# Kernel tuning notes

Hardware: AMD Instinct MI355X
Metric: run time of the kernel (lower is better)

The kernel has to match this reference:

```python
import jax, jax.numpy as jnp
import numpy as np

B, S, D, H, L = 4, 4096, 64, 8, 4
VOCAB, NCLS = 256, 10
MLP = D * H          # mlp_dim = dim * heads = 512
BS = 256             # block size for banded attention
R = 256              # one-sided radius (sliding_window_size = 512)


def sinusoid_pos_emb(s, d):
    pos = np.arange(s)[:, None].astype(np.float32)
    i = np.arange(d // 2)[None, :].astype(np.float32)
    ang = pos / np.power(10000.0, 2.0 * i / d)
    pe = np.zeros((s, d), np.float32)
    pe[:, 0::2] = np.sin(ang)
    pe[:, 1::2] = np.cos(ang)
    return jnp.asarray(pe)


def layernorm(x, s, b):
    m = x.mean(-1, keepdims=True)
    v = ((x - m) ** 2).mean(-1, keepdims=True)
    return (x - m) * jax.lax.rsqrt(v + 1e-6) * s + b


def sliding_window_attn(x, wq, bq, wk, bk, wv, bv, wo, bo):
    Bx, Sx, Dx = x.shape
    Dh = Dx // H
    nb = Sx // BS

    def proj(w, b2):
        return (x @ w + b2).reshape(Bx, Sx, H, Dh).transpose(0, 2, 1, 3)

    q = proj(wq, bq) / jnp.sqrt(jnp.float32(Dh))
    k = proj(wk, bk)
    v = proj(wv, bv)

    def windows(t):  # [B,H,S,Dh] -> [B,H,nb,3*BS,Dh] (prev | self | next blocks)
        tp = jnp.pad(t, ((0, 0), (0, 0), (BS, BS), (0, 0))).reshape(Bx, H, nb + 2, BS, Dh)
        return jnp.concatenate([tp[:, :, :-2], tp[:, :, 1:-1], tp[:, :, 2:]], axis=3)

    kw, vw = windows(k), windows(v)
    qb = q.reshape(Bx, H, nb, BS, Dh)
    scores = jnp.einsum('bhnqd,bhnkd->bhnqk', qb, kw)      # [B,H,nb,BS,3*BS]

    qpos = jnp.arange(BS)[:, None]
    kpos = jnp.arange(3 * BS)[None, :] - BS
    band = jnp.abs(kpos - qpos) <= R                        # [BS,3*BS]
    kglob = jnp.arange(nb)[:, None, None] * BS + kpos[None]  # [nb,1,3*BS]
    valid = (kglob >= 0) & (kglob < Sx)
    mask = band[None] & valid                                # [nb,BS,3*BS]

    scores = jnp.where(mask[None, None], scores, jnp.float32(-1e30))
    probs = jax.nn.softmax(scores, axis=-1)
    out = jnp.einsum('bhnqk,bhnkd->bhnqd', probs, vw)
    out = out.reshape(Bx, H, Sx, Dh).transpose(0, 2, 1, 3).reshape(Bx, Sx, Dx)
    return out @ wo + bo


def setup_inputs() -> dict:
    key = jax.random.key(0)
    ks = jax.random.split(key, 12)
    g = lambda k, shp: jax.random.normal(k, shp, dtype=jnp.float32) * 0.02
    emb = g(ks[0], (VOCAB, D)).at[0].set(0.0)  # padding_idx=0 row is zeros
    return dict(
        x=jax.random.randint(ks[1], (B, S), 0, VOCAB).astype(jnp.int32),
        emb=emb,
        wq=g(ks[2], (L, D, D)), bq=jnp.zeros((L, D)),
        wk=g(ks[3], (L, D, D)), bk=jnp.zeros((L, D)),
        wv=g(ks[4], (L, D, D)), bv=jnp.zeros((L, D)),
        wo=g(ks[5], (L, D, D)), bo=jnp.zeros((L, D)),
        ln1_s=jnp.ones((L, D)), ln1_b=jnp.zeros((L, D)),
        ln2_s=jnp.ones((L, D)), ln2_b=jnp.zeros((L, D)),
        w1=g(ks[6], (L, D, MLP)), b1=jnp.zeros((L, MLP)),
        w2=g(ks[7], (L, MLP, D)), b2=jnp.zeros((L, D)),
        lnf_s=jnp.ones((D,)), lnf_b=jnp.zeros((D,)),
        wcls=g(ks[8], (D, NCLS)), bcls=jnp.zeros((NCLS,)),
    )


def reference(x, emb, wq, bq, wk, bk, wv, bv, wo, bo, ln1_s, ln1_b, ln2_s, ln2_b, w1, b1, w2, b2, lnf_s, lnf_b, wcls, bcls):
    h = emb[x] + sinusoid_pos_emb(S, D)[None]                 # embedding + fixed pos emb
    for l in range(L):
        a = sliding_window_attn(layernorm(h, ln1_s[l], ln1_b[l]),
                                wq[l], bq[l], wk[l], bk[l], wv[l], bv[l], wo[l], bo[l])
        h = h + a
        y = layernorm(h, ln2_s[l], ln2_b[l])
        y = jax.nn.gelu(y @ w1[l] + b1[l]) @ w2[l] + b2[l]
        h = h + y
    h = layernorm(h, lnf_s, lnf_b)
    pooled = h.mean(axis=1)                                   # classifier_pool='MEAN'
    return pooled @ wcls + bcls
```

## Files before the change

### kernel.cpp

```cpp
#include <hip/hip_runtime.h>
#include <hip/hip_bf16.h>

#define DEV __device__ __forceinline__

typedef __attribute__((ext_vector_type(8))) short bf16x8;
typedef __attribute__((ext_vector_type(4))) float f32x4;
typedef __attribute__((ext_vector_type(16))) float f32x16;

DEV short f2bf(float x){ __hip_bfloat16 h = __float2bfloat16(x); return *(short*)&h; }
DEV unsigned pack2bf(float a, float b){
  return (unsigned)(unsigned short)f2bf(a) | ((unsigned)(unsigned short)f2bf(b) << 16);
}
DEV float gelu_fast(float x){
  float z = 0.7978845608028654f*(x + 0.044715f*x*x*x);
  float e = __expf(-2.f*z);
  return x / (1.f + e);
}

#define SB 4096
#define DM 64
#define VSTR 664

__global__ __launch_bounds__(256) void wconv(
    const float* __restrict__ wq, const float* __restrict__ wk,
    const float* __restrict__ wv, const float* __restrict__ wo,
    const float* __restrict__ w1, const float* __restrict__ w2,
    short* __restrict__ wqT, short* __restrict__ wkT,
    short* __restrict__ wvT, short* __restrict__ woT,
    short* __restrict__ w1T, short* __restrict__ w2T)
{
  int t = blockIdx.x, l = blockIdx.y;
  const float* src; short* dst; int K, N, kt, nt;
  if (t < 16) {
    int m = t >> 2, sub = t & 3; kt = sub >> 1; nt = sub & 1; K = 64; N = 64;
    const float* s4[4] = {wq, wk, wv, wo};
    short*       d4[4] = {wqT, wkT, wvT, woT};
    src = s4[m] + l*4096; dst = d4[m] + l*4096;
  } else if (t < 48) {
    kt = (t-16) >> 4; nt = (t-16) & 15; K = 64; N = 512;
    src = w1 + l*32768; dst = w1T + l*32768;
  } else {
    kt = (t-48) >> 1; nt = (t-48) & 1; K = 512; N = 64;
    src = w2 + l*32768; dst = w2T + l*32768;
  }
  __shared__ float lds[32][33];
  int tx = threadIdx.x & 31, ty = threadIdx.x >> 5;
  int k0 = kt*32, n0 = nt*32;
  #pragma unroll
  for (int j=0;j<4;++j) lds[ty+8*j][tx] = src[(size_t)(k0+ty+8*j)*N + n0 + tx];
  __syncthreads();
  #pragma unroll
  for (int j=0;j<4;++j) {
    int nn = ty+8*j;
    dst[(size_t)(n0+nn)*K + k0 + tx] = f2bf(lds[tx][nn]);
  }
}

DEV void make_frags_ln(const float* rowp, float mean, float inv,
    const float* __restrict__ s, const float* __restrict__ b, int kq,
    bf16x8& a0, bf16x8& a1){
  #pragma unroll
  for (int i=0;i<8;++i) a0[i] = f2bf((rowp[kq*8+i]-mean)*inv*s[kq*8+i]+b[kq*8+i]);
  #pragma unroll
  for (int i=0;i<8;++i) a1[i] = f2bf((rowp[32+kq*8+i]-mean)*inv*s[32+kq*8+i]+b[32+kq*8+i]);
}

template<bool EMBED, bool LAST>
__global__ __launch_bounds__(512,2) void fused_kernel(
    const int* __restrict__ x, const float* __restrict__ emb,
    const unsigned short* __restrict__ ab,
    const short* __restrict__ woT, const float* __restrict__ bo,
    const float* __restrict__ ln2s, const float* __restrict__ ln2b,
    const short* __restrict__ w1T, const float* __restrict__ b1,
    const short* __restrict__ w2T, const float* __restrict__ b2,
    const float* __restrict__ lns, const float* __restrict__ lnb,
    const short* __restrict__ wqT, const short* __restrict__ wkT, const short* __restrict__ wvT,
    const float* __restrict__ bq, const float* __restrict__ bk, const float* __restrict__ bv,
    unsigned short* __restrict__ qo, unsigned short* __restrict__ ko, unsigned short* __restrict__ vo,
    float* __restrict__ h, float* __restrict__ part)
{
  __shared__ float hN[64][68];
  __shared__ short mid[64][520];
  __shared__ float facc[64][68];
  __shared__ float mu[64], iv[64];

  const int bid = blockIdx.x;
  const int row_g0 = bid * 64;
  const int tid = threadIdx.x;
  const int w = tid >> 6, lane = tid & 63;
  const int r = lane & 15, kq = lane >> 4;
  const int srow = tid >> 3, sd8 = tid & 7;

  if constexpr (EMBED) {
    int tg = row_g0 + srow;
    int s = tg & (SB-1);
    int tok = x[tg];
    #pragma unroll
    for (int i=0;i<8;++i) {
      int d = sd8*8 + i;
      float fe = (float)(d & ~1) * (1.0f/64.0f);
      float invk = __expf(-9.210340371976184f * fe);
      float ang = (float)s * invk;
      float pe = (d & 1) ? __cosf(ang) : __sinf(ang);
      float val = emb[tok*DM + d] + pe;
      hN[srow][d] = val;
      h[(size_t)tg*DM + d] = val;
    }
  } else {
    const int rh = w >> 2, ct = w & 3;
    const int col = ct*16 + r;
    const short* wp = woT + (size_t)col*64 + kq*8;
    bf16x8 wb0 = *(const bf16x8*)(wp);
    bf16x8 wb1 = *(const bf16x8*)(wp + 32);
    #pragma unroll
    for (int rf=0; rf<2; ++rf) {
      const short* abp = (const short*)(ab + (size_t)(row_g0 + rh*32 + rf*16 + r)*DM + kq*8);
      bf16x8 a0 = *(const bf16x8*)abp;
      bf16x8 a1 = *(const bf16x8*)(abp + 32);
      f32x4 acc = (f32x4){0.f,0.f,0.f,0.f};
      acc = __builtin_amdgcn_mfma_f32_16x16x32_bf16(a0, wb0, acc, 0, 0, 0);
      acc = __builtin_amdgcn_mfma_f32_16x16x32_bf16(a1, wb1, acc, 0, 0, 0);
      #pragma unroll
      for (int j=0;j<4;++j) {
        int rl = rh*32 + rf*16 + kq*4 + j;
        hN[rl][col] = acc[j] + bo[col] + h[(size_t)(row_g0+rl)*DM + col];
      }
    }
  }
  __syncthreads();

  {
    const float* p = &hN[srow][sd8*8];
    float v[8];
    float sum = 0.f;
    #pragma unroll
    for (int i=0;i<8;++i){ v[i] = p[i]; sum += v[i]; }
    sum += __shfl_xor(sum, 1, 64); sum += __shfl_xor(sum, 2, 64); sum += __shfl_xor(sum, 4, 64);
    float mean = sum * (1.f/64.f);
    float sq = 0.f;
    #pragma unroll
    for (int i=0;i<8;++i){ float d = v[i]-mean; sq += d*d; }
    sq += __shfl_xor(sq, 1, 64); sq += __shfl_xor(sq, 2, 64); sq += __shfl_xor(sq, 4, 64);
    if (sd8 == 0) { mu[srow] = mean; iv[srow] = rsqrtf(sq*(1.f/64.f) + 1e-6f); }
  }
  __syncthreads();

  if constexpr (!EMBED) {
    {
      bf16x8 a[4][2];
      #pragma unroll
      for (int rf=0; rf<4; ++rf)
        make_frags_ln(&hN[rf*16 + r][0], mu[rf*16 + r], iv[rf*16 + r], ln2s, ln2b, kq, a[rf][0], a[rf][1]);
      const int gc0 = w*64;
      bf16x8 wb[4][2];
      #pragma unroll
      for (int ct=0; ct<4; ++ct) {
        const short* wp = w1T + (size_t)(gc0 + ct*16 + r)*64 + kq*8;
        wb[ct][0] = *(const bf16x8*)(wp);
        wb[ct][1] = *(const bf16x8*)(wp + 32);
      }
      f32x4 acc1[4][4];
      #pragma unroll
      for (int ct=0;ct<4;++ct)
        #pragma unroll
        for (int rf=0;rf<4;++rf) acc1[ct][rf] = (f32x4){0.f,0.f,0.f,0.f};
      #pragma unroll
      for (int ct=0; ct<4; ++ct)
        #pragma unroll
        for (int rf=0; rf<4; ++rf) {
          acc1[ct][rf] = __builtin_amdgcn_mfma_f32_16x16x32_bf16(a[rf][0], wb[ct][0], acc1[ct][rf], 0, 0, 0);
          acc1[ct][rf] = __builtin_amdgcn_mfma_f32_16x16x32_bf16(a[rf][1], wb[ct][1], acc1[ct][rf], 0, 0, 0);
        }
      #pragma unroll
      for (int ct=0; ct<4; ++ct) {
        int gcol = gc0 + ct*16 + r;
        float bb = b1[gcol];
        #pragma unroll
        for (int rf=0; rf<4; ++rf)
          #pragma unroll
          for (int j=0; j<4; ++j)
            mid[rf*16 + kq*4 + j][gcol] = f2bf(gelu_fast(acc1[ct][rf][j] + bb));
      }
    }
    __syncthreads();

    {
      const int kh = w >> 2, ct2 = w & 3;
      const int col2 = ct2*16 + r;
      bf16x8 wf[8];
      #pragma unroll
      for (int ks=0; ks<8; ++ks)
        wf[ks] = *(const bf16x8*)(w2T + (size_t)col2*512 + kh*256 + ks*32 + kq*8);
      f32x4 acc2[4];
      #pragma unroll
      for (int rf=0;rf<4;++rf) acc2[rf] = (f32x4){0.f,0.f,0.f,0.f};
      #pragma unroll
      for (int ks=0; ks<8; ++ks)
        #pragma unroll
        for (int rf=0; rf<4; ++rf) {
          bf16x8 af = *(const bf16x8*)(&mid[rf*16 + r][kh*256 + ks*32 + kq*8]);
          acc2[rf] = __builtin_amdgcn_mfma_f32_16x16x32_bf16(af, wf[ks], acc2[rf], 0, 0, 0);
        }
      if (kh == 0) {
        #pragma unroll
        for (int rf=0; rf<4; ++rf)
          #pragma unroll
          for (int j=0;j<4;++j)
            facc[rf*16 + kq*4 + j][col2] = acc2[rf][j];
      }
      __syncthreads();
      if (kh == 1) {
        float bb = b2[col2];
        #pragma unroll
        for (int rf=0; rf<4; ++rf)
          #pragma unroll
          for (int j=0;j<4;++j) {
            int rl = rf*16 + kq*4 + j;
            float val = acc2[rf][j] + facc[rl][col2] + bb + hN[rl][col2];
            hN[rl][col2] = val;
            h[(size_t)(row_g0+rl)*DM + col2] = val;
          }
      }
    }
    __syncthreads();

    {
      const float* p = &hN[srow][sd8*8];
      float v[8];
      float sum = 0.f;
      #pragma unroll
      for (int i=0;i<8;++i){ v[i] = p[i]; sum += v[i]; }
      sum += __shfl_xor(sum, 1, 64); sum += __shfl_xor(sum, 2, 64); sum += __shfl_xor(sum, 4, 64);
      float mean = sum * (1.f/64.f);
      float sq = 0.f;
      #pragma unroll
      for (int i=0;i<8;++i){ float d = v[i]-mean; sq += d*d; }
      sq += __shfl_xor(sq, 1, 64); sq += __shfl_xor(sq, 2, 64); sq += __shfl_xor(sq, 4, 64);
      if (sd8 == 0) { mu[srow] = mean; iv[srow] = rsqrtf(sq*(1.f/64.f) + 1e-6f); }
    }
    __syncthreads();
  }

  if constexpr (!LAST) {
    const float qscale = 0.35355339059327373f;
    bf16x8 a[4][2];
    #pragma unroll
    for (int rf=0; rf<4; ++rf)
      make_frags_ln(&hN[rf*16 + r][0], mu[rf*16 + r], iv[rf*16 + r], lns, lnb, kq, a[rf][0], a[rf][1]);
    #pragma unroll
    for (int rep=0; rep<2; ++rep) {
      int jj = w + rep*8;
      if (jj < 12) {
        int m = jj >> 2, ct = jj & 3;
        const short* WT = m==0 ? wqT : (m==1 ? wkT : wvT);
        int col = ct*16 + r;
        const short* wp = WT + (size_t)col*64 + kq*8;
        bf16x8 wb0 = *(const bf16x8*)(wp);
        bf16x8 wb1 = *(const bf16x8*)(wp + 32);
        float bias = (m==0 ? bq : (m==1 ? bk : bv))[col];
        float scale = (m==0) ? qscale : 1.f;
        unsigned short* OPT = m==0 ? qo : (m==1 ? ko : vo);
        #pragma unroll
        for (int rf=0; rf<4; ++rf) {
          f32x4 acc = (f32x4){0.f,0.f,0.f,0.f};
          acc = __builtin_amdgcn_mfma_f32_16x16x32_bf16(a[rf][0], wb0, acc, 0, 0, 0);
          acc = __builtin_amdgcn_mfma_f32_16x16x32_bf16(a[rf][1], wb1, acc, 0, 0, 0);
          #pragma unroll
          for (int j=0;j<4;++j) {
            size_t oi = (size_t)(row_g0 + rf*16 + kq*4 + j)*DM + col;
            OPT[oi] = (unsigned short)f2bf((acc[j] + bias)*scale);
          }
        }
      }
    }
  } else {
    float mean = mu[srow], inv = iv[srow];
    #pragma unroll
    for (int i=0;i<8;++i) {
      int d = sd8*8 + i;
      hN[srow][d] = (hN[srow][d]-mean)*inv*lns[d] + lnb[d];
    }
    __syncthreads();
    if (tid < 64) {
      float s = 0.f;
      #pragma unroll 4
      for (int rr=0; rr<64; ++rr) s += hN[rr][tid];
      part[bid*64 + tid] = s;
    }
  }
}

__global__ __launch_bounds__(256) void attn_kernel(
    const unsigned short* __restrict__ qg_,
    const unsigned short* __restrict__ kg_,
    const unsigned short* __restrict__ vg_,
    __hip_bfloat16* __restrict__ out)
{
  const int qblk = blockIdx.x, bh = blockIdx.y;
  const int b = bh >> 3, hh = bh & 7;
  const int tid = threadIdx.x;
  const int q0b = qblk << 7;
  const int kbase = q0b - 256;

  __shared__ unsigned short Ks[640*8];
  __shared__ unsigned short Vs[8*VSTR];

  const unsigned short* kgp = kg_ + ((size_t)b*SB)*DM + hh*8;
  const unsigned short* vgp = vg_ + ((size_t)b*SB)*DM + hh*8;

  for (int e = tid; e < 640; e += 256) {
    int g = kbase + e;
    uint4 kv = make_uint4(0,0,0,0), vv = make_uint4(0,0,0,0);
    if ((unsigned)g < (unsigned)SB) {
      kv = *(const uint4*)(kgp + (size_t)g*DM);
      vv = *(const uint4*)(vgp + (size_t)g*DM);
    }
    *(uint4*)(Ks + e*8) = kv;
    const unsigned short* pv = (const unsigned short*)&vv;
    #pragma unroll
    for (int d = 0; d < 8; ++d) Vs[d*VSTR + e] = pv[d];
  }
  __syncthreads();

  const int w = tid >> 6;
  const int lane = tid & 63;
  const int qc = lane & 31;
  const int hf = lane >> 5;
  const int qglob = q0b + 32*w + qc;

  bf16x8 qfrag = {};
  if (hf == 0) qfrag = *(const bf16x8*)(qg_ + ((size_t)b*SB + qglob)*DM + hh*8);

  f32x16 oacc = {};
  float lacc = 0.f;

  for (int t = 0; t <= 16; ++t) {
    const int k0l = 32*w + 32*t;
    const int k0g = kbase + k0l;
    if (k0g > SB-1 || k0g + 31 < 0) continue;

    bf16x8 kfrag = {};
    if (hf == 0) kfrag = *(const bf16x8*)(Ks + (k0l + qc)*8);

    f32x16 s = __builtin_amdgcn_mfma_f32_32x32x16_bf16(kfrag, qfrag, (f32x16){}, 0, 0, 0);

    float pp[16];
    bool needmask = (t == 0) | (t == 16) | (k0g < 0) | (k0g + 31 > SB-1);
    if (needmask) {
      #pragma unroll
      for (int rr = 0; rr < 16; ++rr) {
        int klg = k0g + (rr&3) + 8*(rr>>2) + 4*hf;
        bool ok = ((unsigned)(klg - qglob + 256) <= 512u) && ((unsigned)klg < (unsigned)SB);
        pp[rr] = ok ? __expf(s[rr]) : 0.f;
      }
    } else {
      #pragma unroll
      for (int rr = 0; rr < 16; ++rr) pp[rr] = __expf(s[rr]);
    }
    #pragma unroll
    for (int rr = 0; rr < 16; ++rr) lacc += pp[rr];

    unsigned pk[8];
    #pragma unroll
    for (int j = 0; j < 8; ++j) pk[j] = pack2bf(pp[2*j], pp[2*j+1]);
    unsigned sw[8];
    #pragma unroll
    for (int j = 0; j < 8; ++j) sw[j] = __shfl_xor(pk[j], 32, 64);

    union { unsigned u[4]; bf16x8 v; } pb1;
    pb1.u[0] = hf ? sw[2] : pk[0];
    pb1.u[1] = hf ? sw[3] : pk[1];
    pb1.u[2] = hf ? pk[2] : sw[0];
    pb1.u[3] = hf ? pk[3] : sw[1];
    bf16x8 va1 = {};
    if (qc < 8) va1 = *(const bf16x8*)(Vs + qc*VSTR + k0l + 8*hf);
    oacc = __builtin_amdgcn_mfma_f32_32x32x16_bf16(va1, pb1.v, oacc, 0, 0, 0);

    union { unsigned u[4]; bf16x8 v; } pb2;
    pb2.u[0] = hf ? sw[6] : pk[4];
    pb2.u[1] = hf ? sw[7] : pk[5];
    pb2.u[2] = hf ? pk[6] : sw[4];
    pb2.u[3] = hf ? pk[7] : sw[5];
    bf16x8 va2 = {};
    if (qc < 8) va2 = *(const bf16x8*)(Vs + qc*VSTR + k0l + 16 + 8*hf);
    oacc = __builtin_amdgcn_mfma_f32_32x32x16_bf16(va2, pb2.v, oacc, 0, 0, 0);
  }

  float lsum = lacc + __shfl_xor(lacc, 32, 64);
  float rcp = 1.f / lsum;
  unsigned short ov[4];
  #pragma unroll
  for (int j = 0; j < 4; ++j) ov[j] = (unsigned short)f2bf(oacc[j] * rcp);
  *(uint2*)(out + ((size_t)b*SB + qglob)*DM + hh*8 + 4*hf) = *(uint2*)ov;
}

__global__ __launch_bounds__(256) void pool_finalize(const float* __restrict__ part,
    const float* __restrict__ wcls, const float* __restrict__ bcls, float* __restrict__ out)
{
  int tid = threadIdx.x;
  int b = tid >> 6, d = tid & 63;
  float sum = 0.f;
  #pragma unroll 8
  for (int i = 0; i < 64; ++i) sum += part[(b*64 + i)*64 + d];
  __shared__ float pooled[4][64];
  pooled[b][d] = sum * (1.f/4096.f);
  __syncthreads();
  if (tid < 40) {
    int bb = tid / 10, c = tid % 10;
    float acc = bcls[c];
    #pragma unroll
    for (int dd = 0; dd < 64; ++dd) acc = fmaf(pooled[bb][dd], wcls[dd*10 + c], acc);
    out[tid] = acc;
  }
}

extern "C" void kernel_launch(void* const* d_in, const int* in_sizes, int n_in,
                              void* d_out, int out_size, void* d_ws, size_t ws_size,
                              hipStream_t stream)
{
  const int*   x    = (const int*)d_in[0];
  const float* emb  = (const float*)d_in[1];
  const float* wq   = (const float*)d_in[2];
  const float* bq   = (const float*)d_in[3];
  const float* wk   = (const float*)d_in[4];
  const float* bk   = (const float*)d_in[5];
  const float* wv   = (const float*)d_in[6];
  const float* bv   = (const float*)d_in[7];
  const float* wo   = (const float*)d_in[8];
  const float* bo   = (const float*)d_in[9];
  const float* ln1s = (const float*)d_in[10];
  const float* ln1b = (const float*)d_in[11];
  const float* ln2s = (const float*)d_in[12];
  const float* ln2b = (const float*)d_in[13];
  const float* w1   = (const float*)d_in[14];
  const float* b1   = (const float*)d_in[15];
  const float* w2   = (const float*)d_in[16];
  const float* b2   = (const float*)d_in[17];
  const float* lnfs = (const float*)d_in[18];
  const float* lnfb = (const float*)d_in[19];
  const float* wcls = (const float*)d_in[20];
  const float* bcls = (const float*)d_in[21];
  float* out = (float*)d_out;

  char* wsb = (char*)d_ws;
  const size_t MB = 1u << 20;
  float* h  = (float*)(wsb);
  unsigned short* qb2 = (unsigned short*)(wsb + 4*MB);
  unsigned short* kb2 = (unsigned short*)(wsb + 6*MB);
  unsigned short* vb2 = (unsigned short*)(wsb + 8*MB);
  unsigned short* ab  = (unsigned short*)(wsb + 10*MB);
  short* wqT = (short*)(wsb + 12*MB);
  short* wkT = (short*)(wsb + 12*MB + 32*1024);
  short* wvT = (short*)(wsb + 12*MB + 64*1024);
  short* woT = (short*)(wsb + 12*MB + 96*1024);
  short* w1T = (short*)(wsb + 12*MB + 128*1024);
  short* w2T = (short*)(wsb + 12*MB + 384*1024);
  float* part = (float*)(wsb + 13*MB);

  wconv<<<dim3(80,4),256,0,stream>>>(wq,wk,wv,wo,w1,w2, wqT,wkT,wvT,woT,w1T,w2T);

  fused_kernel<true,false><<<256,512,0,stream>>>(
      x, emb, nullptr,
      nullptr, nullptr, nullptr, nullptr,
      nullptr, nullptr, nullptr, nullptr,
      ln1s, ln1b,
      wqT, wkT, wvT, bq, bk, bv,
      qb2, kb2, vb2, h, nullptr);

  for (int l = 0; l < 4; ++l) {
    attn_kernel<<<dim3(32,32),256,0,stream>>>(qb2, kb2, vb2, (__hip_bfloat16*)ab);
    if (l < 3) {
      fused_kernel<false,false><<<256,512,0,stream>>>(
          nullptr, nullptr, ab,
          woT+4096*l, bo+64*l, ln2s+64*l, ln2b+64*l,
          w1T+32768*l, b1+512*l, w2T+32768*l, b2+64*l,
          ln1s+64*(l+1), ln1b+64*(l+1),
          wqT+4096*(l+1), wkT+4096*(l+1), wvT+4096*(l+1),
          bq+64*(l+1), bk+64*(l+1), bv+64*(l+1),
          qb2, kb2, vb2, h, nullptr);
    } else {
      fused_kernel<false,true><<<256,512,0,stream>>>(
          nullptr, nullptr, ab,
          woT+4096*l, bo+64*l, ln2s+64*l, ln2b+64*l,
          w1T+32768*l, b1+512*l, w2T+32768*l, b2+64*l,
          lnfs, lnfb,
          nullptr, nullptr, nullptr, nullptr, nullptr, nullptr,
          nullptr, nullptr, nullptr, h, part);
    }
  }
  pool_finalize<<<1,256,0,stream>>>(part, wcls, bcls, out);
}
```

Baseline: 204.3 us.

## Fuse sliding-window attention into the per-layer fused kernel with ping-pong QKV buffers

Removes the separate attention kernel and computes banded attention for each 64-row tile inside the layer kernel. Each block loads a 576-row K/V window for all 8 heads into shared memory, and each wave handles one head. The attention output stays in LDS and feeds the output projection directly, so the global round-trip through the attention buffer and one launch per layer are gone. Q/K/V are double-buffered across layers to avoid read/write hazards. The cost is reused LDS regions, an extra barrier, and only 256 blocks of work that each recompute a wide K/V window, which lowers parallelism for the attention part.

```diff
diff --git a/kernel.cpp b/kernel.cpp
--- a/kernel.cpp
+++ b/kernel.cpp
@@ -18,8 +18,8 @@
 }
 
 #define SB 4096
+#define NT 16384
 #define DM 64
-#define VSTR 664
 
 __global__ __launch_bounds__(256) void wconv(
     const float* __restrict__ wq, const float* __restrict__ wk,
@@ -66,9 +66,10 @@
 }
 
 template<bool EMBED, bool LAST>
-__global__ __launch_bounds__(512,2) void fused_kernel(
+__global__ __launch_bounds__(512,2) void layer_kernel(
     const int* __restrict__ x, const float* __restrict__ emb,
-    const unsigned short* __restrict__ ab,
+    const unsigned short* __restrict__ qin, const unsigned short* __restrict__ kin,
+    const unsigned short* __restrict__ vin,
     const short* __restrict__ woT, const float* __restrict__ bo,
     const float* __restrict__ ln2s, const float* __restrict__ ln2b,
     const short* __restrict__ w1T, const float* __restrict__ b1,
@@ -79,10 +80,16 @@
     unsigned short* __restrict__ qo, unsigned short* __restrict__ ko, unsigned short* __restrict__ vo,
     float* __restrict__ h, float* __restrict__ part)
 {
-  __shared__ float hN[64][68];
-  __shared__ short mid[64][520];
-  __shared__ float facc[64][68];
+  __shared__ uint4 regA4[4608];
+  __shared__ uint4 regB4[4672];
   __shared__ float mu[64], iv[64];
+
+  unsigned short* Ks  = (unsigned short*)regA4;
+  unsigned short* abL = (unsigned short*)regA4;
+  float (*hN)[68]   = (float(*)[68])((char*)regA4 + 9216);
+  float (*facc)[68] = (float(*)[68])((char*)regA4 + 26624);
+  unsigned short* Vs = (unsigned short*)regB4;
+  short (*mid)[520]  = (short(*)[520])regB4;
 
   const int bid = blockIdx.x;
   const int row_g0 = bid * 64;
@@ -107,23 +114,125 @@
       h[(size_t)tg*DM + d] = val;
     }
   } else {
-    const int rh = w >> 2, ct = w & 3;
-    const int col = ct*16 + r;
-    const short* wp = woT + (size_t)col*64 + kq*8;
-    bf16x8 wb0 = *(const bf16x8*)(wp);
-    bf16x8 wb1 = *(const bf16x8*)(wp + 32);
-    #pragma unroll
-    for (int rf=0; rf<2; ++rf) {
-      const short* abp = (const short*)(ab + (size_t)(row_g0 + rh*32 + rf*16 + r)*DM + kq*8);
-      bf16x8 a0 = *(const bf16x8*)abp;
-      bf16x8 a1 = *(const bf16x8*)(abp + 32);
-      f32x4 acc = (f32x4){0.f,0.f,0.f,0.f};
-      acc = __builtin_amdgcn_mfma_f32_16x16x32_bf16(a0, wb0, acc, 0, 0, 0);
-      acc = __builtin_amdgcn_mfma_f32_16x16x32_bf16(a1, wb1, acc, 0, 0, 0);
-      #pragma unroll
-      for (int j=0;j<4;++j) {
-        int rl = rh*32 + rf*16 + kq*4 + j;
-        hN[rl][col] = acc[j] + bo[col] + h[(size_t)(row_g0+rl)*DM + col];
+    const int bbase = row_g0 & ~(SB-1);
+    const int kwin0 = row_g0 - 256;
+
+    for (int idx = tid; idx < 4608; idx += 512) {
+      int e = idx >> 3, grp = idx & 7;
+      int g = kwin0 + e;
+      uint4 kv = make_uint4(0,0,0,0), vv = make_uint4(0,0,0,0);
+      if ((unsigned)(g - bbase) < (unsigned)SB) {
+        kv = *(const uint4*)(kin + (size_t)g*DM + grp*8);
+        vv = *(const uint4*)(vin + (size_t)g*DM + grp*8);
+      }
+      *(uint4*)(Ks + e*64 + ((grp ^ (e & 7)) << 3)) = kv;
+      const unsigned short* pv = (const unsigned short*)&vv;
+      #pragma unroll
+      for (int d = 0; d < 8; ++d) Vs[(grp*8 + d)*584 + e] = pv[d];
+    }
+    __syncthreads();
+
+    const int qc = lane & 31;
+    const int hf = lane >> 5;
+
+    auto attn_job = [&](int qs, f32x16& oacc, float& lacc) {
+      const int qglob = row_g0 + qs*32 + qc;
+      bf16x8 qfrag = {};
+      if (hf == 0) qfrag = *(const bf16x8*)(qin + (size_t)qglob*DM + w*8);
+      for (int t = 0; t <= 16; ++t) {
+        const int k0l = qs*32 + 32*t;
+        const int k0g = kwin0 + k0l;
+        if (k0g > bbase + SB-1 || k0g + 31 < bbase) continue;
+
+        bf16x8 kfrag = {};
+        if (hf == 0) {
+          int e = k0l + qc;
+          kfrag = *(const bf16x8*)(Ks + e*64 + ((w ^ (e & 7)) << 3));
+        }
+        f32x16 s = __builtin_amdgcn_mfma_f32_32x32x16_bf16(kfrag, qfrag, (f32x16){}, 0, 0, 0);
+
+        float pp[16];
+        bool needmask = (t == 0) | (t == 16) | (k0g < bbase) | (k0g + 31 > bbase + SB-1);
+        if (needmask) {
+          #pragma unroll
+          for (int rr = 0; rr < 16; ++rr) {
+            int klg = k0g + (rr&3) + 8*(rr>>2) + 4*hf;
+            bool ok = ((unsigned)(klg - qglob + 256) <= 512u) &&
+                      ((unsigned)(klg - bbase) < (unsigned)SB);
+            pp[rr] = ok ? __expf(s[rr]) : 0.f;
+          }
+        } else {
+          #pragma unroll
+          for (int rr = 0; rr < 16; ++rr) pp[rr] = __expf(s[rr]);
+        }
+        #pragma unroll
+        for (int rr = 0; rr < 16; ++rr) lacc += pp[rr];
+
+        unsigned pk[8];
+        #pragma unroll
+        for (int j = 0; j < 8; ++j) pk[j] = pack2bf(pp[2*j], pp[2*j+1]);
+        unsigned sw[8];
+        #pragma unroll
+        for (int j = 0; j < 8; ++j) sw[j] = __shfl_xor(pk[j], 32, 64);
+
+        union { unsigned u[4]; bf16x8 v; } pbA;
+        pbA.u[0] = hf ? sw[2] : pk[0];
+        pbA.u[1] = hf ? sw[3] : pk[1];
+        pbA.u[2] = hf ? pk[2] : sw[0];
+        pbA.u[3] = hf ? pk[3] : sw[1];
+        bf16x8 va1 = {};
+        if (qc < 8) va1 = *(const bf16x8*)(Vs + (w*8 + qc)*584 + k0l + 8*hf);
+        oacc = __builtin_amdgcn_mfma_f32_32x32x16_bf16(va1, pbA.v, oacc, 0, 0, 0);
+
+        union { unsigned u[4]; bf16x8 v; } pbB;
+        pbB.u[0] = hf ? sw[6] : pk[4];
+        pbB.u[1] = hf ? sw[7] : pk[5];
+        pbB.u[2] = hf ? pk[6] : sw[4];
+        pbB.u[3] = hf ? pk[7] : sw[5];
+        bf16x8 va2 = {};
+        if (qc < 8) va2 = *(const bf16x8*)(Vs + (w*8 + qc)*584 + k0l + 16 + 8*hf);
+        oacc = __builtin_amdgcn_mfma_f32_32x32x16_bf16(va2, pbB.v, oacc, 0, 0, 0);
+      }
+    };
+
+    f32x16 oacc0 = {}; float la0 = 0.f;
+    f32x16 oacc1 = {}; float la1 = 0.f;
+    attn_job(0, oacc0, la0);
+    attn_job(1, oacc1, la1);
+    float rcp0 = 1.f / (la0 + __shfl_xor(la0, 32, 64));
+    float rcp1 = 1.f / (la1 + __shfl_xor(la1, 32, 64));
+    __syncthreads();
+
+    {
+      unsigned short ov[4];
+      #pragma unroll
+      for (int j = 0; j < 4; ++j) ov[j] = (unsigned short)f2bf(oacc0[j] * rcp0);
+      *(uint2*)(abL + (qc)*72 + w*8 + 4*hf) = *(uint2*)ov;
+      #pragma unroll
+      for (int j = 0; j < 4; ++j) ov[j] = (unsigned short)f2bf(oacc1[j] * rcp1);
+      *(uint2*)(abL + (32 + qc)*72 + w*8 + 4*hf) = *(uint2*)ov;
+    }
+    __syncthreads();
+
+    {
+      const int rh = w >> 2, ct = w & 3;
+      const int col = ct*16 + r;
+      const short* wp = woT + (size_t)col*64 + kq*8;
+      bf16x8 wb0 = *(const bf16x8*)(wp);
+      bf16x8 wb1 = *(const bf16x8*)(wp + 32);
+      #pragma unroll
+      for (int rf=0; rf<2; ++rf) {
+        const short* abp = (const short*)(abL + (rh*32 + rf*16 + r)*72 + kq*8);
+        bf16x8 a0 = *(const bf16x8*)abp;
+        bf16x8 a1 = *(const bf16x8*)(abp + 32);
+        f32x4 acc = (f32x4){0.f,0.f,0.f,0.f};
+        acc = __builtin_amdgcn_mfma_f32_16x16x32_bf16(a0, wb0, acc, 0, 0, 0);
+        acc = __builtin_amdgcn_mfma_f32_16x16x32_bf16(a1, wb1, acc, 0, 0, 0);
+        #pragma unroll
+        for (int j=0;j<4;++j) {
+          int rl = rh*32 + rf*16 + kq*4 + j;
+          hN[rl][col] = acc[j] + bo[col] + h[(size_t)(row_g0+rl)*DM + col];
+        }
       }
     }
   }
@@ -171,6 +280,7 @@
           acc1[ct][rf] = __builtin_amdgcn_mfma_f32_16x16x32_bf16(a[rf][0], wb[ct][0], acc1[ct][rf], 0, 0, 0);
           acc1[ct][rf] = __builtin_amdgcn_mfma_f32_16x16x32_bf16(a[rf][1], wb[ct][1], acc1[ct][rf], 0, 0, 0);
         }
+      __syncthreads();
       #pragma unroll
       for (int ct=0; ct<4; ++ct) {
         int gcol = gc0 + ct*16 + r;
@@ -288,110 +398,6 @@
       part[bid*64 + tid] = s;
     }
   }
-}
-
-__global__ __launch_bounds__(256) void attn_kernel(
-    const unsigned short* __restrict__ qg_,
-    const unsigned short* __restrict__ kg_,
-    const unsigned short* __restrict__ vg_,
-    __hip_bfloat16* __restrict__ out)
-{
-  const int qblk = blockIdx.x, bh = blockIdx.y;
-  const int b = bh >> 3, hh = bh & 7;
-  const int tid = threadIdx.x;
-  const int q0b = qblk << 7;
-  const int kbase = q0b - 256;
-
-  __shared__ unsigned short Ks[640*8];
-  __shared__ unsigned short Vs[8*VSTR];
-
-  const unsigned short* kgp = kg_ + ((size_t)b*SB)*DM + hh*8;
-  const unsigned short* vgp = vg_ + ((size_t)b*SB)*DM + hh*8;
-
-  for (int e = tid; e < 640; e += 256) {
-    int g = kbase + e;
-    uint4 kv = make_uint4(0,0,0,0), vv = make_uint4(0,0,0,0);
-    if ((unsigned)g < (unsigned)SB) {
-      kv = *(const uint4*)(kgp + (size_t)g*DM);
-      vv = *(const uint4*)(vgp + (size_t)g*DM);
-    }
-    *(uint4*)(Ks + e*8) = kv;
-    const unsigned short* pv = (const unsigned short*)&vv;
-    #pragma unroll
-    for (int d = 0; d < 8; ++d) Vs[d*VSTR + e] = pv[d];
-  }
-  __syncthreads();
-
-  const int w = tid >> 6;
-  const int lane = tid & 63;
-  const int qc = lane & 31;
-  const int hf = lane >> 5;
-  const int qglob = q0b + 32*w + qc;
-
-  bf16x8 qfrag = {};
-  if (hf == 0) qfrag = *(const bf16x8*)(qg_ + ((size_t)b*SB + qglob)*DM + hh*8);
-
-  f32x16 oacc = {};
-  float lacc = 0.f;
-
-  for (int t = 0; t <= 16; ++t) {
-    const int k0l = 32*w + 32*t;
-    const int k0g = kbase + k0l;
-    if (k0g > SB-1 || k0g + 31 < 0) continue;
-
-    bf16x8 kfrag = {};
-    if (hf == 0) kfrag = *(const bf16x8*)(Ks + (k0l + qc)*8);
-
-    f32x16 s = __builtin_amdgcn_mfma_f32_32x32x16_bf16(kfrag, qfrag, (f32x16){}, 0, 0, 0);
-
-    float pp[16];
-    bool needmask = (t == 0) | (t == 16) | (k0g < 0) | (k0g + 31 > SB-1);
-    if (needmask) {
-      #pragma unroll
-      for (int rr = 0; rr < 16; ++rr) {
-        int klg = k0g + (rr&3) + 8*(rr>>2) + 4*hf;
-        bool ok = ((unsigned)(klg - qglob + 256) <= 512u) && ((unsigned)klg < (unsigned)SB);
-        pp[rr] = ok ? __expf(s[rr]) : 0.f;
-      }
-    } else {
-      #pragma unroll
-      for (int rr = 0; rr < 16; ++rr) pp[rr] = __expf(s[rr]);
-    }
-    #pragma unroll
-    for (int rr = 0; rr < 16; ++rr) lacc += pp[rr];
-
-    unsigned pk[8];
-    #pragma unroll
-    for (int j = 0; j < 8; ++j) pk[j] = pack2bf(pp[2*j], pp[2*j+1]);
-    unsigned sw[8];
-    #pragma unroll
-    for (int j = 0; j < 8; ++j) sw[j] = __shfl_xor(pk[j], 32, 64);
-
-    union { unsigned u[4]; bf16x8 v; } pb1;
-    pb1.u[0] = hf ? sw[2] : pk[0];
-    pb1.u[1] = hf ? sw[3] : pk[1];
-    pb1.u[2] = hf ? pk[2] : sw[0];
-    pb1.u[3] = hf ? pk[3] : sw[1];
-    bf16x8 va1 = {};
-    if (qc < 8) va1 = *(const bf16x8*)(Vs + qc*VSTR + k0l + 8*hf);
-    oacc = __builtin_amdgcn_mfma_f32_32x32x16_bf16(va1, pb1.v, oacc, 0, 0, 0);
-
-    union { unsigned u[4]; bf16x8 v; } pb2;
-    pb2.u[0] = hf ? sw[6] : pk[4];
-    pb2.u[1] = hf ? sw[7] : pk[5];
-    pb2.u[2] = hf ? pk[6] : sw[4];
-    pb2.u[3] = hf ? pk[7] : sw[5];
-    bf16x8 va2 = {};
-    if (qc < 8) va2 = *(const bf16x8*)(Vs + qc*VSTR + k0l + 16 + 8*hf);
-    oacc = __builtin_amdgcn_mfma_f32_32x32x16_bf16(va2, pb2.v, oacc, 0, 0, 0);
-  }
-
-  float lsum = lacc + __shfl_xor(lacc, 32, 64);
-  float rcp = 1.f / lsum;
-  unsigned short ov[4];
-  #pragma unroll
-  for (int j = 0; j < 4; ++j) ov[j] = (unsigned short)f2bf(oacc[j] * rcp);
-  *(uint2*)(out + ((size_t)b*SB + qglob)*DM + hh*8 + 4*hf) = *(uint2*)ov;
 }
 
 __global__ __launch_bounds__(256) void pool_finalize(const float* __restrict__ part,
@@ -445,42 +451,49 @@
   char* wsb = (char*)d_ws;
   const size_t MB = 1u << 20;
   float* h  = (float*)(wsb);
-  unsigned short* qb2 = (unsigned short*)(wsb + 4*MB);
-  unsigned short* kb2 = (unsigned short*)(wsb + 6*MB);
-  unsigned short* vb2 = (unsigned short*)(wsb + 8*MB);
-  unsigned short* ab  = (unsigned short*)(wsb + 10*MB);
-  short* wqT = (short*)(wsb + 12*MB);
-  short* wkT = (short*)(wsb + 12*MB + 32*1024);
-  short* wvT = (short*)(wsb + 12*MB + 64*1024);
-  short* woT = (short*)(wsb + 12*MB + 96*1024);
-  short* w1T = (short*)(wsb + 12*MB + 128*1024);
-  short* w2T = (short*)(wsb + 12*MB + 384*1024);
-  float* part = (float*)(wsb + 13*MB);
+  unsigned short* qA = (unsigned short*)(wsb + 4*MB);
+  unsigned short* kA = (unsigned short*)(wsb + 6*MB);
+  unsigned short* vA = (unsigned short*)(wsb + 8*MB);
+  unsigned short* qB = (unsigned short*)(wsb + 10*MB);
+  unsigned short* kB = (unsigned short*)(wsb + 12*MB);
+  unsigned short* vB = (unsigned short*)(wsb + 14*MB);
+  short* wqT = (short*)(wsb + 16*MB);
+  short* wkT = (short*)(wsb + 16*MB + 32*1024);
+  short* wvT = (short*)(wsb + 16*MB + 64*1024);
+  short* woT = (short*)(wsb + 16*MB + 96*1024);
+  short* w1T = (short*)(wsb + 16*MB + 128*1024);
+  short* w2T = (short*)(wsb + 16*MB + 384*1024);
+  float* part = (float*)(wsb + 17*MB);
 
   wconv<<<dim3(80,4),256,0,stream>>>(wq,wk,wv,wo,w1,w2, wqT,wkT,wvT,woT,w1T,w2T);
 
-  fused_kernel<true,false><<<256,512,0,stream>>>(
-      x, emb, nullptr,
+  layer_kernel<true,false><<<256,512,0,stream>>>(
+      x, emb, nullptr, nullptr, nullptr,
       nullptr, nullptr, nullptr, nullptr,
       nullptr, nullptr, nullptr, nullptr,
       ln1s, ln1b,
       wqT, wkT, wvT, bq, bk, bv,
-      qb2, kb2, vb2, h, nullptr);
+      qA, kA, vA, h, nullptr);
 
   for (int l = 0; l < 4; ++l) {
-    attn_kernel<<<dim3(32,32),256,0,stream>>>(qb2, kb2, vb2, (__hip_bfloat16*)ab);
+    unsigned short* qi = (l & 1) ? qB : qA;
+    unsigned short* ki = (l & 1) ? kB : kA;
+    unsigned short* vi = (l & 1) ? vB : vA;
+    unsigned short* qu = (l & 1) ? qA : qB;
+    unsigned short* ku = (l & 1) ? kA : kB;
+    unsigned short* vu = (l & 1) ? vA : vB;
     if (l < 3) {
-      fused_kernel<false,false><<<256,512,0,stream>>>(
-          nullptr, nullptr, ab,
+      layer_kernel<false,false><<<256,512,0,stream>>>(
+          nullptr, nullptr, qi, ki, vi,
           woT+4096*l, bo+64*l, ln2s+64*l, ln2b+64*l,
           w1T+32768*l, b1+512*l, w2T+32768*l, b2+64*l,
           ln1s+64*(l+1), ln1b+64*(l+1),
           wqT+4096*(l+1), wkT+4096*(l+1), wvT+4096*(l+1),
           bq+64*(l+1), bk+64*(l+1), bv+64*(l+1),
-          qb2, kb2, vb2, h, nullptr);
+          qu, ku, vu, h, nullptr);
     } else {
-      fused_kernel<false,true><<<256,512,0,stream>>>(
-          nullptr, nullptr, ab,
+      layer_kernel<false,true><<<256,512,0,stream>>>(
+          nullptr, nullptr, qi, ki, vi,
           woT+4096*l, bo+64*l, ln2s+64*l, ln2b+64*l,
           w1T+32768*l, b1+512*l, w2T+32768*l, b2+64*l,
           lnfs, lnfb,
```

New measurement: 184.3 us. 9.8% less time.
